# Optimization experiments

Hardware: AMD Instinct MI355X
Metric: run time of the kernel (lower is better)

Reference implementation:

```python
import jax, jax.numpy as jnp
import numpy as np

N_IN = 100000
N_OUT = 100000
E = 1600000
C_IN = 1
C_MID = 64
C_OUT = 64
POS_DIM = 3


def setup_inputs() -> dict:
    key = jax.random.key(0)
    ks = jax.random.split(key, 10)
    x_in = jax.random.normal(ks[0], (N_IN, C_IN), dtype=jnp.float32)
    pos_in = jax.random.uniform(ks[1], (N_IN, POS_DIM), dtype=jnp.float32)
    batch_in = jnp.zeros((N_IN,), dtype=jnp.int64)
    pos_out = jax.random.uniform(ks[2], (N_OUT, POS_DIM), dtype=jnp.float32)
    in_index = jax.random.randint(ks[3], (E,), 0, N_IN, dtype=jnp.int64)
    out_index = jnp.sort(jax.random.randint(ks[4], (E,), 0, N_OUT, dtype=jnp.int64))
    # parameters (Linear weights stored as [in, out] for x @ W)
    s1 = 1.0 / np.sqrt(POS_DIM)
    s2 = 1.0 / np.sqrt(16)
    s3 = 1.0 / np.sqrt(C_MID * C_IN)
    W1 = jax.random.uniform(ks[5], (POS_DIM, 16), dtype=jnp.float32, minval=-s1, maxval=s1)
    W2 = jax.random.uniform(ks[6], (16, C_MID), dtype=jnp.float32, minval=-s2, maxval=s2)
    W3 = jax.random.uniform(ks[7], (C_MID * C_IN, C_OUT), dtype=jnp.float32, minval=-s3, maxval=s3)
    b3 = jax.random.uniform(ks[8], (C_OUT,), dtype=jnp.float32, minval=-s3, maxval=s3)
    return {"x_in": x_in, "pos_in": pos_in, "batch_in": batch_in, "pos_out": pos_out,
            "in_index": in_index, "out_index": out_index,
            "W1": W1, "W2": W2, "W3": W3, "b3": b3}


def reference(x_in, pos_in, batch_in, pos_out, in_index, out_index, W1, W2, W3, b3):
    n_out = pos_out.shape[0]
    # gather relative positions per edge: [E, pos_dim]
    pos_local = pos_in[in_index] - pos_out[out_index]
    # per-edge MLP on geometry
    M = jax.nn.celu(pos_local @ W1)          # [E, 16]
    M = jax.nn.celu(M @ W2)                  # [E, c_mid]
    # gather node features per edge
    x_edge = x_in[in_index]                  # [E, c_in]
    # degree normalization (clamped to >= 1)
    deg = jax.ops.segment_sum(jnp.ones((out_index.shape[0],), dtype=pos_in.dtype),
                              out_index, num_segments=n_out)
    deg = jnp.maximum(deg, 1.0)
    x_edge = x_edge / deg[out_index][:, None]
    # outer product and scatter-sum into output nodes
    outer = jnp.einsum('ei,ej->eij', x_edge, M)  # [E, c_in, c_mid]
    agg = jax.ops.segment_sum(outer.reshape(outer.shape[0], -1), out_index,
                              num_segments=n_out)  # [N_out, c_in*c_mid]
    out = agg @ W3 + b3
    out = jnp.nan_to_num(out, nan=0.0, posinf=1e6, neginf=-1e6)
    return out
```

## Files before the change

### kernel.cpp

```cpp
#include <hip/hip_runtime.h>
#include <math.h>


typedef __attribute__((ext_vector_type(8))) short short8;
typedef __attribute__((ext_vector_type(4))) float f32x4;
typedef __attribute__((ext_vector_type(4))) int   int4v;
typedef __attribute__((ext_vector_type(2))) int   int2v;

union frag_u { int i[4]; short8 v; };

__device__ __forceinline__ float celu1(float x) {
    float m = fminf(x, 0.0f);
    return fmaxf(x, __expf(m) - 1.0f);
}
__device__ __forceinline__ int cvt_pk_bf16(float lo, float hi) {
    int r; asm("v_cvt_pk_bf16_f32 %0, %1, %2" : "=v"(r) : "v"(lo), "v"(hi)); return r;
}

__global__ void k_zero_start(const int* __restrict__ oi, int* __restrict__ start,
                             f32x4* __restrict__ agg4, int n_out, int E, int nzero4,
                             const float* __restrict__ pos_in,
                             const float* __restrict__ x_in,
                             f32x4* __restrict__ pos4, int n_in,
                             const float* __restrict__ pos_out,
                             f32x4* __restrict__ pos_out4) {
    const int t = blockIdx.x * blockDim.x + threadIdx.x;
    if (t <= E) {
        const int cur  = (t < E) ? oi[t] : n_out;
        const int prev = (t > 0) ? oi[t - 1] : -1;
        for (int o = prev + 1; o <= cur; ++o) start[o] = t;
    }
    if (pos4 != nullptr && t < n_in) {
        f32x4 v;
        v.x = pos_in[t*3+0]; v.y = pos_in[t*3+1]; v.z = pos_in[t*3+2];
        v.w = x_in[t];
        pos4[t] = v;
    }
    if (pos_out4 != nullptr && t < n_out) {
        f32x4 v;
        v.x = pos_out[t*3+0]; v.y = pos_out[t*3+1]; v.z = pos_out[t*3+2];
        v.w = 0.0f;
        pos_out4[t] = v;
    }
    const f32x4 z = {0.f, 0.f, 0.f, 0.f};
    for (int i = t; i < nzero4; i += gridDim.x * blockDim.x) agg4[i] = z;
}

template<int TIER>
__global__ __launch_bounds__(256, 6) void k_edges(
    const float* __restrict__ x_in, const float* __restrict__ pos_in,
    const f32x4* __restrict__ pos4, const f32x4* __restrict__ pos_out4,
    const float* __restrict__ pos_out, const int* __restrict__ in_index,
    const int* __restrict__ out_index,
    const float* __restrict__ W1, const float* __restrict__ W2,
    float* __restrict__ agg, int E, int nwin, int totwaves)
{
    __shared__ int   hbuf [4][64][10];
    __shared__ float scoef[4][64];
    __shared__ int   srank[4][64];
    __shared__ int   snid [4][64];
    __shared__ int   snidw[4][16];

    const int wv = threadIdx.x >> 6, lane = threadIdx.x & 63;
    const int kcol = lane & 15, q = lane >> 4;

    frag_u b1[4];
#pragma unroll
    for (int jt = 0; jt < 4; ++jt) {
        const int j = jt * 16 + kcol;
        b1[jt].i[0] = cvt_pk_bf16(W2[(4*q+0)*64 + j], W2[(4*q+1)*64 + j]);
        b1[jt].i[1] = cvt_pk_bf16(W2[(4*q+2)*64 + j], W2[(4*q+3)*64 + j]);
        b1[jt].i[2] = 0; b1[jt].i[3] = 0;
    }
    const f32x4 zero4 = {0.f, 0.f, 0.f, 0.f};

    for (int win = blockIdx.x * 4 + wv; win < nwin; win += totwaves) {
        const int e = win * 64 + lane;
        const bool valid = e < E;
        const int ec = valid ? e : E - 1;

        const int node = out_index[ec];
        const int idx  = in_index[ec];

        float xv, pix, piy, piz;
        if (TIER >= 1) {
            const f32x4 pv = pos4[idx];
            pix = pv.x; piy = pv.y; piz = pv.z; xv = pv.w;
        } else {
            xv  = x_in[idx];
            pix = pos_in[idx*3+0]; piy = pos_in[idx*3+1]; piz = pos_in[idx*3+2];
        }
        float pox, poy, poz;
        if (TIER >= 2) {
            const f32x4 po = pos_out4[node];
            pox = po.x; poy = po.y; poz = po.z;
        } else {
            pox = pos_out[node*3+0]; poy = pos_out[node*3+1]; poz = pos_out[node*3+2];
        }
        const float coef = valid ? xv : 0.0f;
        const float px = pix - pox;
        const float py = piy - poy;
        const float pz = piz - poz;

        int hp[8];
#pragma unroll
        for (int c = 0; c < 8; ++c) {
            const float h0 = celu1(fmaf(pz, W1[32 + 2*c],     fmaf(py, W1[16 + 2*c],     px * W1[2*c])));
            const float h1 = celu1(fmaf(pz, W1[32 + 2*c + 1], fmaf(py, W1[16 + 2*c + 1], px * W1[2*c + 1])));
            hp[c] = cvt_pk_bf16(h0, h1);
        }
        *(int4v*)&hbuf[wv][lane][0] = *(const int4v*)&hp[0];
        *(int4v*)&hbuf[wv][lane][4] = *(const int4v*)&hp[4];

        const int prevn = __shfl_up(node, 1);
        const bool whead = (lane == 0) || (node != prevn);
        const unsigned long long wbal = __ballot(whead);
        const int ndw = __popcll(wbal);

        scoef[wv][lane] = coef;

        if (ndw <= 16) {
            const int wrank = __popcll(wbal & ((2ULL << lane) - 1)) - 1;
            srank[wv][lane] = wrank;
            if (whead) snidw[wv][wrank] = node;

            f32x4 d2acc[4] = {zero4, zero4, zero4, zero4};

#pragma unroll
            for (int Q = 0; Q < 4; ++Q) {
                const int2v a1lo = *(const int2v*)&hbuf[wv][Q*16 + kcol][2*q];
                frag_u a1; a1.i[0] = a1lo.x; a1.i[1] = a1lo.y; a1.i[2] = 0; a1.i[3] = 0;

                const f32x4 c4 = *(const f32x4*)&scoef[wv][Q*16 + 4*q];
                const int4v r4 = *(const int4v*)&srank[wv][Q*16 + 4*q];

                frag_u a2;
                a2.i[0] = cvt_pk_bf16(r4.x == kcol ? c4.x : 0.0f, r4.y == kcol ? c4.y : 0.0f);
                a2.i[1] = cvt_pk_bf16(r4.z == kcol ? c4.z : 0.0f, r4.w == kcol ? c4.w : 0.0f);
                a2.i[2] = 0; a2.i[3] = 0;

#pragma unroll
                for (int jt = 0; jt < 4; ++jt) {
                    f32x4 d1 = __builtin_amdgcn_mfma_f32_16x16x32_bf16(a1.v, b1[jt].v, zero4, 0, 0, 0);
                    frag_u b2;
                    b2.i[0] = cvt_pk_bf16(celu1(d1[0]), celu1(d1[1]));
                    b2.i[1] = cvt_pk_bf16(celu1(d1[2]), celu1(d1[3]));
                    b2.i[2] = 0; b2.i[3] = 0;
                    d2acc[jt] = __builtin_amdgcn_mfma_f32_16x16x32_bf16(a2.v, b2.v, d2acc[jt], 0, 0, 0);
                }
            }

            const int4v n4 = *(const int4v*)&snidw[wv][4*q & 15];
            float* p0 = agg + (long)n4.x * 64 + kcol;
            float* p1 = agg + (long)n4.y * 64 + kcol;
            float* p2 = agg + (long)n4.z * 64 + kcol;
            float* p3 = agg + (long)n4.w * 64 + kcol;
#pragma unroll
            for (int jt = 0; jt < 4; ++jt) {
                if (4*q + 0 < ndw) unsafeAtomicAdd(p0 + jt * 16, d2acc[jt][0]);
                if (4*q + 1 < ndw) unsafeAtomicAdd(p1 + jt * 16, d2acc[jt][1]);
                if (4*q + 2 < ndw) unsafeAtomicAdd(p2 + jt * 16, d2acc[jt][2]);
                if (4*q + 3 < ndw) unsafeAtomicAdd(p3 + jt * 16, d2acc[jt][3]);
            }
        } else {
            const unsigned long long qbal = wbal | 0x0001000100010001ULL;
            const unsigned mym = (unsigned)(qbal >> (q * 16)) & 0xFFFFu;
            const int rank = __popc(mym & ((2u << kcol) - 1)) - 1;
            srank[wv][lane] = rank;
            const bool qhead = (qbal >> lane) & 1ull;
            if (qhead) snid[wv][(lane & 48) + rank] = node;

            int ndq[4];
#pragma unroll
            for (int Q = 0; Q < 4; ++Q) ndq[Q] = __popc((unsigned)(qbal >> (Q * 16)) & 0xFFFFu);

#pragma unroll
            for (int Q = 0; Q < 4; ++Q) {
                const int2v a1lo = *(const int2v*)&hbuf[wv][Q*16 + kcol][2*q];
                frag_u a1; a1.i[0] = a1lo.x; a1.i[1] = a1lo.y; a1.i[2] = 0; a1.i[3] = 0;

                const f32x4 c4 = *(const f32x4*)&scoef[wv][Q*16 + 4*q];
                const int4v r4 = *(const int4v*)&srank[wv][Q*16 + 4*q];
                const int4v n4 = *(const int4v*)&snid [wv][Q*16 + 4*q];

                frag_u a2;
                a2.i[0] = cvt_pk_bf16(r4.x == kcol ? c4.x : 0.0f, r4.y == kcol ? c4.y : 0.0f);
                a2.i[1] = cvt_pk_bf16(r4.z == kcol ? c4.z : 0.0f, r4.w == kcol ? c4.w : 0.0f);
                a2.i[2] = 0; a2.i[3] = 0;

                const int nd = ndq[Q];
                float* p0 = agg + (long)n4.x * 64 + kcol;
                float* p1 = agg + (long)n4.y * 64 + kcol;
                float* p2 = agg + (long)n4.z * 64 + kcol;
                float* p3 = agg + (long)n4.w * 64 + kcol;

#pragma unroll
                for (int jt = 0; jt < 4; ++jt) {
                    f32x4 d1 = __builtin_amdgcn_mfma_f32_16x16x32_bf16(a1.v, b1[jt].v, zero4, 0, 0, 0);
                    frag_u b2;
                    b2.i[0] = cvt_pk_bf16(celu1(d1[0]), celu1(d1[1]));
                    b2.i[1] = cvt_pk_bf16(celu1(d1[2]), celu1(d1[3]));
                    b2.i[2] = 0; b2.i[3] = 0;
                    f32x4 d2 = __builtin_amdgcn_mfma_f32_16x16x32_bf16(a2.v, b2.v, zero4, 0, 0, 0);
                    if (4*q + 0 < nd) unsafeAtomicAdd(p0 + jt * 16, d2[0]);
                    if (4*q + 1 < nd) unsafeAtomicAdd(p1 + jt * 16, d2[1]);
                    if (4*q + 2 < nd) unsafeAtomicAdd(p2 + jt * 16, d2[2]);
                    if (4*q + 3 < nd) unsafeAtomicAdd(p3 + jt * 16, d2[3]);
                }
            }
        }
    }
}

__global__ __launch_bounds__(256) void k_out(
    float* __restrict__ agg, const float* __restrict__ W3,
    const float* __restrict__ b3, const int* __restrict__ start,
    int n_out, int ntiles, int totwaves)
{
    const int wv = threadIdx.x >> 6, lane = threadIdx.x & 63;
    const int s = lane & 15, q = lane >> 4;

    frag_u B0[4], B1[4];
    float bias[4];
#pragma unroll
    for (int jt = 0; jt < 4; ++jt) {
        const int j = jt * 16 + s;
        bias[jt] = b3[j];
        B0[jt].i[0] = cvt_pk_bf16(W3[( 4*q+0)*64+j], W3[( 4*q+1)*64+j]);
        B0[jt].i[1] = cvt_pk_bf16(W3[( 4*q+2)*64+j], W3[( 4*q+3)*64+j]);
        B0[jt].i[2] = cvt_pk_bf16(W3[(16+4*q+0)*64+j], W3[(16+4*q+1)*64+j]);
        B0[jt].i[3] = cvt_pk_bf16(W3[(16+4*q+2)*64+j], W3[(16+4*q+3)*64+j]);
        B1[jt].i[0] = cvt_pk_bf16(W3[(32+4*q+0)*64+j], W3[(32+4*q+1)*64+j]);
        B1[jt].i[1] = cvt_pk_bf16(W3[(32+4*q+2)*64+j], W3[(32+4*q+3)*64+j]);
        B1[jt].i[2] = cvt_pk_bf16(W3[(48+4*q+0)*64+j], W3[(48+4*q+1)*64+j]);
        B1[jt].i[3] = cvt_pk_bf16(W3[(48+4*q+2)*64+j], W3[(48+4*q+3)*64+j]);
    }
    const f32x4 zero4 = {0.f, 0.f, 0.f, 0.f};

    for (int tile = blockIdx.x * 4 + wv; tile < ntiles; tile += totwaves) {
        const long base = (long)tile * 16;

        const long row_i = base + s;
        const long row_c = row_i < n_out ? row_i : n_out - 1;
        const float* row = agg + row_c * 64;
        const int dd = start[row_c + 1] - start[row_c];
        const float invd = 1.0f / (float)(dd > 0 ? dd : 1);

        f32x4 r0 = *(const f32x4*)(row +      4*q);
        f32x4 r1 = *(const f32x4*)(row + 16 + 4*q);
        f32x4 r2 = *(const f32x4*)(row + 32 + 4*q);
        f32x4 r3 = *(const f32x4*)(row + 48 + 4*q);
        r0 *= invd; r1 *= invd; r2 *= invd; r3 *= invd;

        frag_u A0, A1;
        A0.i[0] = cvt_pk_bf16(r0.x, r0.y); A0.i[1] = cvt_pk_bf16(r0.z, r0.w);
        A0.i[2] = cvt_pk_bf16(r1.x, r1.y); A0.i[3] = cvt_pk_bf16(r1.z, r1.w);
        A1.i[0] = cvt_pk_bf16(r2.x, r2.y); A1.i[1] = cvt_pk_bf16(r2.z, r2.w);
        A1.i[2] = cvt_pk_bf16(r3.x, r3.y); A1.i[3] = cvt_pk_bf16(r3.z, r3.w);

#pragma unroll
        for (int jt = 0; jt < 4; ++jt) {
            f32x4 d = __builtin_amdgcn_mfma_f32_16x16x32_bf16(A0.v, B0[jt].v, zero4, 0, 0, 0);
            d = __builtin_amdgcn_mfma_f32_16x16x32_bf16(A1.v, B1[jt].v, d, 0, 0, 0);
            const int j = jt * 16 + s;
#pragma unroll
            for (int r = 0; r < 4; ++r) {
                const long nodei = base + 4*q + r;
                if (nodei < n_out) {
                    float v = d[r] + bias[jt];
                    if (isnan(v)) v = 0.0f;
                    else if (isinf(v)) v = (v > 0.0f) ? 1e6f : -1e6f;
                    agg[nodei * 64 + j] = v;
                }
            }
        }
    }
}

extern "C" void kernel_launch(void* const* d_in, const int* in_sizes, int n_in_args,
                              void* d_out, int out_size, void* d_ws, size_t ws_size,
                              hipStream_t stream) {
    const float* x_in      = (const float*)d_in[0];
    const float* pos_in    = (const float*)d_in[1];
    const float* pos_out   = (const float*)d_in[3];
    const int*   in_index  = (const int*)d_in[4];
    const int*   out_index = (const int*)d_in[5];
    const float* W1        = (const float*)d_in[6];
    const float* W2        = (const float*)d_in[7];
    const float* W3        = (const float*)d_in[8];
    const float* b3        = (const float*)d_in[9];
    float* out = (float*)d_out;

    const int n_out = in_sizes[3] / 3;
    const int E     = in_sizes[4];
    const int n_in  = in_sizes[0];

    int* start = (int*)d_ws;
    const size_t start_bytes = ((size_t)(n_out + 1) * 4 + 255) & ~(size_t)255;
    const size_t need1 = start_bytes + (size_t)n_in * 16;
    const size_t need2 = need1 + (size_t)n_out * 16;
    const int tier = (ws_size >= need2) ? 2 : (ws_size >= need1 ? 1 : 0);
    f32x4* pos4    = tier >= 1 ? (f32x4*)((char*)d_ws + start_bytes) : nullptr;
    f32x4* pos_out4= tier >= 2 ? (f32x4*)((char*)d_ws + need1) : nullptr;

    {
        const int nzero4 = n_out * 16;
        int span = (E + 1) > nzero4 ? (E + 1) : nzero4;
        if (n_in > span) span = n_in;
        dim3 b(256), g((span + 255) / 256);
        k_zero_start<<<g, b, 0, stream>>>(out_index, start, (f32x4*)out, n_out, E,
                                          nzero4, pos_in, x_in, pos4, n_in,
                                          pos_out, pos_out4);
    }

    {
        const int nwin = (E + 63) / 64;
        const int nblocks = (nwin + 3) / 4;
        const int totwaves = nblocks * 4;
        if (tier == 2)
            k_edges<2><<<dim3(nblocks), dim3(256), 0, stream>>>(
                x_in, pos_in, pos4, pos_out4, pos_out, in_index, out_index, W1, W2, out, E, nwin, totwaves);
        else if (tier == 1)
            k_edges<1><<<dim3(nblocks), dim3(256), 0, stream>>>(
                x_in, pos_in, pos4, pos_out4, pos_out, in_index, out_index, W1, W2, out, E, nwin, totwaves);
        else
            k_edges<0><<<dim3(nblocks), dim3(256), 0, stream>>>(
                x_in, pos_in, pos4, pos_out4, pos_out, in_index, out_index, W1, W2, out, E, nwin, totwaves);
    }
    {
        const int ntiles = (n_out + 15) / 16;
        const int nblocks = (ntiles + 7) / 8;
        const int totwaves = nblocks * 4;
        k_out<<<dim3(nblocks), dim3(256), 0, stream>>>(
            out, W3, b3, start, n_out, ntiles, totwaves);
    }
}
```

Baseline: 66.14 us.

## Partition edge kernel by output-node groups using segment start offsets

Each wave now owns a group of 16 output nodes and walks the edge range from the start array, instead of taking fixed 64-edge windows in a grid-stride loop. Boundaries between waves then line up with node segments, which can cut contention on the scatter into agg (atomics at window boundaries), depending on the unseen body. The cost is uneven work per wave, because degrees vary, and partially filled last windows in each group, which adds masked lanes.

```diff
diff --git a/kernel.cpp b/kernel.cpp
--- a/kernel.cpp
+++ b/kernel.cpp
@@ -53,7 +53,8 @@
     const float* __restrict__ pos_out, const int* __restrict__ in_index,
     const int* __restrict__ out_index,
     const float* __restrict__ W1, const float* __restrict__ W2,
-    float* __restrict__ agg, int E, int nwin, int totwaves)
+    const int* __restrict__ start,
+    float* __restrict__ agg, int E, int n_out, int ngroups)
 {
     __shared__ int   hbuf [4][64][10];
     __shared__ float scoef[4][64];
@@ -74,10 +75,17 @@
     }
     const f32x4 zero4 = {0.f, 0.f, 0.f, 0.f};
 
-    for (int win = blockIdx.x * 4 + wv; win < nwin; win += totwaves) {
-        const int e = win * 64 + lane;
-        const bool valid = e < E;
-        const int ec = valid ? e : E - 1;
+    const int g = blockIdx.x * 4 + wv;
+    if (g >= ngroups) return;
+    const int base = g * 16;
+    const int hi   = (base + 16 <= n_out) ? base + 16 : n_out;
+    const int gs = start[base];
+    const int ge = start[hi];
+
+    for (int w0 = gs; w0 < ge; w0 += 64) {
+        const int e = w0 + lane;
+        const bool valid = e < ge;
+        const int ec = valid ? e : ge - 1;
 
         const int node = out_index[ec];
         const int idx  = in_index[ec];
@@ -300,8 +308,8 @@
     const size_t need1 = start_bytes + (size_t)n_in * 16;
     const size_t need2 = need1 + (size_t)n_out * 16;
     const int tier = (ws_size >= need2) ? 2 : (ws_size >= need1 ? 1 : 0);
-    f32x4* pos4    = tier >= 1 ? (f32x4*)((char*)d_ws + start_bytes) : nullptr;
-    f32x4* pos_out4= tier >= 2 ? (f32x4*)((char*)d_ws + need1) : nullptr;
+    f32x4* pos4     = tier >= 1 ? (f32x4*)((char*)d_ws + start_bytes) : nullptr;
+    f32x4* pos_out4 = tier >= 2 ? (f32x4*)((char*)d_ws + need1) : nullptr;
 
     {
         const int nzero4 = n_out * 16;
@@ -314,18 +322,20 @@
     }
 
     {
-        const int nwin = (E + 63) / 64;
-        const int nblocks = (nwin + 3) / 4;
-        const int totwaves = nblocks * 4;
+        const int ngroups = (n_out + 15) / 16;
+        const int nblocks = (ngroups + 3) / 4;
         if (tier == 2)
             k_edges<2><<<dim3(nblocks), dim3(256), 0, stream>>>(
-                x_in, pos_in, pos4, pos_out4, pos_out, in_index, out_index, W1, W2, out, E, nwin, totwaves);
+                x_in, pos_in, pos4, pos_out4, pos_out, in_index, out_index,
+                W1, W2, start, out, E, n_out, ngroups);
         else if (tier == 1)
             k_edges<1><<<dim3(nblocks), dim3(256), 0, stream>>>(
-                x_in, pos_in, pos4, pos_out4, pos_out, in_index, out_index, W1, W2, out, E, nwin, totwaves);
+                x_in, pos_in, pos4, pos_out4, pos_out, in_index, out_index,
+                W1, W2, start, out, E, n_out, ngroups);
         else
             k_edges<0><<<dim3(nblocks), dim3(256), 0, stream>>>(
-                x_in, pos_in, pos4, pos_out4, pos_out, in_index, out_index, W1, W2, out, E, nwin, totwaves);
+                x_in, pos_in, pos4, pos_out4, pos_out, in_index, out_index,
+                W1, W2, start, out, E, n_out, ngroups);
     }
     {
         const int ntiles = (n_out + 15) / 16;
```

After: 80.06 us. +21.1%, slower.
